# Kernel tuning notes

Measured on AMD Instinct MI355X. Metric: run time of the kernel, lower is better.

## Reference

```python
import jax, jax.numpy as jnp
import numpy as np

# ---- static config (decode path of PagedAttention) ----
B = 16            # batch (one new token per sequence in decode)
H = 32            # query heads
KVH = 8           # kv heads (GQA)
G = H // KVH      # query heads per kv head group
D = 128           # head dim (Rope hard-codes split at 64)
BLOCK = 16        # block_size hard-coded in forward
CACHE_LEN = 4096  # cache_length[b] for every b (uniform)
NUM_FETCH = CACHE_LEN // BLOCK          # 256 full blocks fetched per seq
MAX_BLOCKS = B * (NUM_FETCH + 1)        # 4112; one spare block per seq
ROWS = MAX_BLOCKS * BLOCK               # 65792 flat cache rows
SCALE = 1.0 / np.sqrt(D)                # softmax_scale


def setup_inputs() -> dict:
    key = jax.random.key(0)
    ks = jax.random.split(key, 6)
    Q = jax.random.normal(ks[0], (B, H, D), jnp.float32)
    K = jax.random.normal(ks[1], (B, KVH, D), jnp.float32)
    V = jax.random.normal(ks[2], (B, KVH, D), jnp.float32)
    Kcache = jax.random.normal(ks[3], (ROWS, KVH, D), jnp.float32)
    Vcache = jax.random.normal(ks[4], (ROWS, KVH, D), jnp.float32)
    # rotary cos/sin for the current decode position (one per sequence)
    inv_freq = 1.0 / (10000.0 ** (jnp.arange(D // 2, dtype=jnp.float32) / (D // 2)))
    pos = jnp.full((B, 1), float(CACHE_LEN), dtype=jnp.float32)
    ang = pos * inv_freq[None, :]                      # [B, 64]
    cos = jnp.concatenate([jnp.cos(ang), jnp.cos(ang)], axis=-1)  # [B, 128]
    sin = jnp.concatenate([jnp.sin(ang), jnp.sin(ang)], axis=-1)
    # block-aligned page table: seq b owns blocks [b*257, b*257+256)
    fetch_slots = ((jnp.arange(B, dtype=jnp.int32)[:, None] * (NUM_FETCH + 1)
                    + jnp.arange(NUM_FETCH, dtype=jnp.int32)[None, :]) * BLOCK)
    save_slots = ((jnp.arange(B, dtype=jnp.int32) * (NUM_FETCH + 1) + NUM_FETCH)
                  * BLOCK).reshape(B, 1)
    return dict(Q=Q, K=K, V=V, Kcache=Kcache, Vcache=Vcache,
                cos=cos, sin=sin, fetch_slots=fetch_slots, save_slots=save_slots)


def _rope(x, cos, sin):
    # x: [B, heads, 128]; matches torch: x*cos + concat(-x2, x1)*sin
    x1, x2 = x[..., :D // 2], x[..., D // 2:]
    rot = jnp.concatenate([-x2, x1], axis=-1)
    return x * cos[:, None, :] + rot * sin[:, None, :]


def reference(Q, K, V, Kcache, Vcache, cos, sin, fetch_slots, save_slots):
    Qr = _rope(Q, cos, sin)          # [B, H, D]
    Kr = _rope(K, cos, sin)          # [B, KVH, D]
    # cache physical per-block layout is [kv_heads, block, d]
    Kc4 = Kcache.reshape(MAX_BLOCKS, KVH, BLOCK, D)
    Vc4 = Vcache.reshape(MAX_BLOCKS, KVH, BLOCK, D)
    blk = fetch_slots // BLOCK                         # [B, NUM_FETCH]
    # paged gather: [B, NF, KVH, BLOCK, D] -> [B, KVH, CACHE_LEN, D]
    Kb = jnp.transpose(Kc4[blk], (0, 2, 1, 3, 4)).reshape(B, KVH, CACHE_LEN, D)
    Vb = jnp.transpose(Vc4[blk], (0, 2, 1, 3, 4)).reshape(B, KVH, CACHE_LEN, D)
    # append the new (roped) K and raw V token -> N = CACHE_LEN + 1
    Kall = jnp.concatenate([Kb, Kr[:, :, None, :]], axis=2)
    Vall = jnp.concatenate([Vb, V[:, :, None, :]], axis=2)
    # torch's tile-repeat maps query head h -> kv head h % KVH;
    # reshape [B, G, KVH, D] puts head g*KVH+k at [g, k], kv index k. Exact match.
    Qg = Qr.reshape(B, G, KVH, D)
    scores = jnp.einsum('bgkd,bknd->bgkn', Qg, Kall) * SCALE   # [B,G,KVH,N]
    p = jax.nn.softmax(scores, axis=-1)
    Yg = jnp.einsum('bgkn,bknd->bgkd', p, Vall)                # [B,G,KVH,D]
    Y = Yg.reshape(B, H, D)
    # scatter-write of new K/V into save_slots (in-place cache update in torch;
    # does not affect Y since save blocks are disjoint from fetch blocks)
    # Kc4.at[save_slots[:,0]//BLOCK, :, save_slots[:,0]%BLOCK, :].set(Kr)
    return Y


if __name__ == '__main__':
    out = reference(**setup_inputs())
    print(out.shape, out.dtype)
```

## Files before the change

kernel.cpp:

```cpp
#include <hip/hip_runtime.h>

#define NB 16
#define NH 32
#define NKVH 8
#define NG 4
#define ND 128
#define BLOCK 16
#define NUM_FETCH 256
#define NSPLIT 16
#define CHUNK 256
#define ITERS 32

static constexpr float SCALE_LOG2E = 0.08838834764831845f * 1.4426950408889634f;


__global__ __launch_bounds__(256, 4) void pa_main(
    const float* __restrict__ Q,
    const float* __restrict__ Kcache,
    const float* __restrict__ Vcache,
    const float* __restrict__ cosb,
    const float* __restrict__ sinb,
    const int*   __restrict__ fetch,
    float* __restrict__ accws,
    float* __restrict__ lws)
{
    const int wg    = blockIdx.x;
    const int split = wg & (NSPLIT - 1);
    const int kvh   = (wg >> 4) & (NKVH - 1);
    const int b     = wg >> 7;

    const int tid  = threadIdx.x;
    const int w    = tid >> 6;
    const int lane = tid & 63;
    const int half = lane >> 5;
    const int l32  = lane & 31;
    const int d0   = l32 << 2;

    const float4 cs = *(const float4*)(cosb + b * ND + d0);
    const float4 sn = *(const float4*)(sinb + b * ND + d0);
    const float  sgn = (d0 < 64) ? -1.f : 1.f;
    const int    dp  = d0 ^ 64;
    float qv[NG][4];
    #pragma unroll
    for (int g = 0; g < NG; ++g) {
        const float* qp = Q + (size_t)(b * NH + g * NKVH + kvh) * ND;
        const float4 qa = *(const float4*)(qp + d0);
        const float4 qb = *(const float4*)(qp + dp);
        qv[g][0] = (qa.x * cs.x + sgn * qb.x * sn.x) * SCALE_LOG2E;
        qv[g][1] = (qa.y * cs.y + sgn * qb.y * sn.y) * SCALE_LOG2E;
        qv[g][2] = (qa.z * cs.z + sgn * qb.z * sn.z) * SCALE_LOG2E;
        qv[g][3] = (qa.w * cs.w + sgn * qb.w * sn.w) * SCALE_LOG2E;
    }

    float acc[NG][4] = {{0.f,0.f,0.f,0.f},{0.f,0.f,0.f,0.f},
                        {0.f,0.f,0.f,0.f},{0.f,0.f,0.f,0.f}};
    float lsum[NG] = {0.f, 0.f, 0.f, 0.f};

    const int   pos0  = split * CHUNK + w * 2 + half;
    const int* __restrict__ fbase = fetch + b * NUM_FETCH;
    const size_t khead = (size_t)kvh * (BLOCK * ND);
    const float* kb = Kcache + khead + d0;
    const float* vb = Vcache + khead + d0;

    #pragma unroll 2
    for (int it = 0; it < ITERS; ++it) {
        const int pos = pos0 + it * 8;
        const size_t off = (size_t)fbase[pos >> 4] * (NKVH * ND)
                         + (size_t)(pos & (BLOCK - 1)) * ND;
        const float4 k4 = *(const float4*)(kb + off);
        const float4 v4 = *(const float4*)(vb + off);

        float s[NG];
        #pragma unroll
        for (int g = 0; g < NG; ++g)
            s[g] = qv[g][0]*k4.x + qv[g][1]*k4.y + qv[g][2]*k4.z + qv[g][3]*k4.w;

        #pragma unroll
        for (int m = 16; m >= 1; m >>= 1) {
            #pragma unroll
            for (int g = 0; g < NG; ++g)
                s[g] += __shfl_xor(s[g], m, 64);
        }

        #pragma unroll
        for (int g = 0; g < NG; ++g) {
            const float p = __builtin_amdgcn_exp2f(s[g]);
            lsum[g]   += p;
            acc[g][0] += p * v4.x;
            acc[g][1] += p * v4.y;
            acc[g][2] += p * v4.z;
            acc[g][3] += p * v4.w;
        }
    }

    #pragma unroll
    for (int g = 0; g < NG; ++g) {
        lsum[g] += __shfl_xor(lsum[g], 32, 64);
        #pragma unroll
        for (int j = 0; j < 4; ++j)
            acc[g][j] += __shfl_xor(acc[g][j], 32, 64);
    }

    __shared__ float s_acc[4][NG][ND];
    __shared__ float s_l[4][NG];
    if (half == 0) {
        #pragma unroll
        for (int g = 0; g < NG; ++g)
            *(float4*)&s_acc[w][g][d0] =
                make_float4(acc[g][0], acc[g][1], acc[g][2], acc[g][3]);
        if (l32 == 0) {
            #pragma unroll
            for (int g = 0; g < NG; ++g) s_l[w][g] = lsum[g];
        }
    }
    __syncthreads();

    const size_t pslot = (size_t)(b * NKVH + kvh) * NSPLIT + split;
    for (int idx = tid; idx < NG * ND; idx += 256) {
        const int g = idx >> 7, d = idx & 127;
        accws[(pslot * NG + g) * ND + d] =
            s_acc[0][g][d] + s_acc[1][g][d] + s_acc[2][g][d] + s_acc[3][g][d];
    }
    if (tid < NG)
        lws[pslot * NG + tid] = s_l[0][tid] + s_l[1][tid] + s_l[2][tid] + s_l[3][tid];
}

__global__ __launch_bounds__(128) void pa_combine(
    const float* __restrict__ Q,
    const float* __restrict__ Knew,
    const float* __restrict__ Vnew,
    const float* __restrict__ cosb,
    const float* __restrict__ sinb,
    const float* __restrict__ accws,
    const float* __restrict__ lws,
    float* __restrict__ Y)
{
    const int bh  = blockIdx.x;
    const int b   = bh >> 5;
    const int h   = bh & (NH - 1);
    const int kvh = h & (NKVH - 1);
    const int g   = h >> 3;
    const int d   = threadIdx.x;

    const float c   = cosb[b * ND + d];
    const float s   = sinb[b * ND + d];
    const float sgn = (d < 64) ? -1.f : 1.f;
    const int   dp  = d ^ 64;
    const float* qp = Q    + (size_t)(b * NH + h) * ND;
    const float* kp = Knew + (size_t)(b * NKVH + kvh) * ND;
    const float qr = qp[d] * c + sgn * qp[dp] * s;
    const float kr = kp[d] * c + sgn * kp[dp] * s;

    float prod = qr * kr;
    #pragma unroll
    for (int m = 32; m >= 1; m >>= 1) prod += __shfl_xor(prod, m, 64);
    __shared__ float red[2];
    if ((d & 63) == 0) red[d >> 6] = prod;
    __syncthreads();

    const float p = __builtin_amdgcn_exp2f((red[0] + red[1]) * SCALE_LOG2E);

    const size_t base = ((size_t)(b * NKVH + kvh) * NSPLIT) * NG + g;
    float acc = p * Vnew[(size_t)(b * NKVH + kvh) * ND + d];
    float lt  = p;
    #pragma unroll
    for (int sp = 0; sp < NSPLIT; ++sp) {
        acc += accws[(base + (size_t)sp * NG) * ND + d];
        lt  += lws[base + (size_t)sp * NG];
    }
    Y[(size_t)(b * NH + h) * ND + d] = acc / lt;
}

extern "C" void kernel_launch(void* const* d_in, const int* in_sizes, int n_in,
                              void* d_out, int out_size, void* d_ws, size_t ws_size,
                              hipStream_t stream)
{
    const float* Q    = (const float*)d_in[0];
    const float* K    = (const float*)d_in[1];
    const float* V    = (const float*)d_in[2];
    const float* Kc   = (const float*)d_in[3];
    const float* Vc   = (const float*)d_in[4];
    const float* cosb = (const float*)d_in[5];
    const float* sinb = (const float*)d_in[6];
    const int*   fetch = (const int*)d_in[7];

    float* accws = (float*)d_ws;
    float* lws   = accws + (size_t)NB * NKVH * NSPLIT * NG * ND;
    float* Y     = (float*)d_out;

    pa_main<<<NB * NKVH * NSPLIT, 256, 0, stream>>>(Q, Kc, Vc, cosb, sinb, fetch, accws, lws);
    pa_combine<<<NB * NH, 128, 0, stream>>>(Q, K, V, cosb, sinb, accws, lws, Y);
}
```

Before: 102.6 us.

## Software-pipeline paged K/V loads two pages ahead with scalar page indices

```diff
diff --git a/kernel.cpp b/kernel.cpp
--- a/kernel.cpp
+++ b/kernel.cpp
@@ -8,8 +8,7 @@
 #define BLOCK 16
 #define NUM_FETCH 256
 #define NSPLIT 16
-#define CHUNK 256
-#define ITERS 32
+#define PAGES_PER_WG 16
 
 static constexpr float SCALE_LOG2E = 0.08838834764831845f * 1.4426950408889634f;
 
@@ -36,6 +35,8 @@
     const int l32  = lane & 31;
     const int d0   = l32 << 2;
 
+    const int* fb = fetch + b * NUM_FETCH + split * PAGES_PER_WG;
+
     const float4 cs = *(const float4*)(cosb + b * ND + d0);
     const float4 sn = *(const float4*)(sinb + b * ND + d0);
     const float  sgn = (d0 < 64) ? -1.f : 1.f;
@@ -56,32 +57,22 @@
                         {0.f,0.f,0.f,0.f},{0.f,0.f,0.f,0.f}};
     float lsum[NG] = {0.f, 0.f, 0.f, 0.f};
 
-    const int   pos0  = split * CHUNK + w * 2 + half;
-    const int* __restrict__ fbase = fetch + b * NUM_FETCH;
+    const int sub = w * 2 + half;
     const size_t khead = (size_t)kvh * (BLOCK * ND);
-    const float* kb = Kcache + khead + d0;
-    const float* vb = Vcache + khead + d0;
-
-    #pragma unroll 2
-    for (int it = 0; it < ITERS; ++it) {
-        const int pos = pos0 + it * 8;
-        const size_t off = (size_t)fbase[pos >> 4] * (NKVH * ND)
-                         + (size_t)(pos & (BLOCK - 1)) * ND;
-        const float4 k4 = *(const float4*)(kb + off);
-        const float4 v4 = *(const float4*)(vb + off);
-
+    const float* kb = Kcache + khead + (size_t)sub * ND + d0;
+    const float* vb = Vcache + khead + (size_t)sub * ND + d0;
+
+    auto body = [&](const float4& k4, const float4& v4) {
         float s[NG];
         #pragma unroll
         for (int g = 0; g < NG; ++g)
             s[g] = qv[g][0]*k4.x + qv[g][1]*k4.y + qv[g][2]*k4.z + qv[g][3]*k4.w;
-
         #pragma unroll
         for (int m = 16; m >= 1; m >>= 1) {
             #pragma unroll
             for (int g = 0; g < NG; ++g)
                 s[g] += __shfl_xor(s[g], m, 64);
         }
-
         #pragma unroll
         for (int g = 0; g < NG; ++g) {
             const float p = __builtin_amdgcn_exp2f(s[g]);
@@ -91,6 +82,36 @@
             acc[g][2] += p * v4.z;
             acc[g][3] += p * v4.w;
         }
+    };
+
+    const int pgA = __builtin_amdgcn_readfirstlane(fb[0]);
+    const int pgB = __builtin_amdgcn_readfirstlane(fb[1]);
+    const size_t offA = (size_t)pgA * (NKVH * ND);
+    const size_t offB = (size_t)pgB * (NKVH * ND);
+    float4 kA0 = *(const float4*)(kb + offA);
+    float4 kA1 = *(const float4*)(kb + offA + 8 * ND);
+    float4 vA0 = *(const float4*)(vb + offA);
+    float4 vA1 = *(const float4*)(vb + offA + 8 * ND);
+    float4 kB0 = *(const float4*)(kb + offB);
+    float4 kB1 = *(const float4*)(kb + offB + 8 * ND);
+    float4 vB0 = *(const float4*)(vb + offB);
+    float4 vB1 = *(const float4*)(vb + offB + 8 * ND);
+
+    #pragma unroll 2
+    for (int j = 0; j < PAGES_PER_WG; ++j) {
+        const int jn = (j + 2 < PAGES_PER_WG) ? (j + 2) : (PAGES_PER_WG - 1);
+        const int pgC = __builtin_amdgcn_readfirstlane(fb[jn]);
+        const size_t offC = (size_t)pgC * (NKVH * ND);
+        const float4 kC0 = *(const float4*)(kb + offC);
+        const float4 kC1 = *(const float4*)(kb + offC + 8 * ND);
+        const float4 vC0 = *(const float4*)(vb + offC);
+        const float4 vC1 = *(const float4*)(vb + offC + 8 * ND);
+
+        body(kA0, vA0);
+        body(kA1, vA1);
+
+        kA0 = kB0; kA1 = kB1; vA0 = vB0; vA1 = vB1;
+        kB0 = kC0; kB1 = kC1; vB0 = vC0; vB1 = vC1;
     }
 
     #pragma unroll
```

After: 105.6 us. 2.9% more time.

## Restructure decode loop to page-major tiles with four rows per half-wave

Applied to the files above, without the earlier changes.

```diff
diff --git a/kernel.cpp b/kernel.cpp
--- a/kernel.cpp
+++ b/kernel.cpp
@@ -7,9 +7,9 @@
 #define ND 128
 #define BLOCK 16
 #define NUM_FETCH 256
-#define NSPLIT 16
-#define CHUNK 256
-#define ITERS 32
+#define NSPLIT 32
+#define PAGES_PER_WG 8
+#define ITERS 4
 
 static constexpr float SCALE_LOG2E = 0.08838834764831845f * 1.4426950408889634f;
 
@@ -26,8 +26,8 @@
 {
     const int wg    = blockIdx.x;
     const int split = wg & (NSPLIT - 1);
-    const int kvh   = (wg >> 4) & (NKVH - 1);
-    const int b     = wg >> 7;
+    const int kvh   = (wg >> 5) & (NKVH - 1);
+    const int b     = wg >> 8;
 
     const int tid  = threadIdx.x;
     const int w    = tid >> 6;
@@ -35,6 +35,10 @@
     const int half = lane >> 5;
     const int l32  = lane & 31;
     const int d0   = l32 << 2;
+
+    const int* fb = fetch + b * NUM_FETCH + split * PAGES_PER_WG;
+    const int  ps = w >> 1;
+    const int  r0 = ((w & 1) * 2 + half) * 4;
 
     const float4 cs = *(const float4*)(cosb + b * ND + d0);
     const float4 sn = *(const float4*)(sinb + b * ND + d0);
@@ -56,40 +60,57 @@
                         {0.f,0.f,0.f,0.f},{0.f,0.f,0.f,0.f}};
     float lsum[NG] = {0.f, 0.f, 0.f, 0.f};
 
-    const int   pos0  = split * CHUNK + w * 2 + half;
-    const int* __restrict__ fbase = fetch + b * NUM_FETCH;
-    const size_t khead = (size_t)kvh * (BLOCK * ND);
-    const float* kb = Kcache + khead + d0;
-    const float* vb = Vcache + khead + d0;
-
-    #pragma unroll 2
-    for (int it = 0; it < ITERS; ++it) {
-        const int pos = pos0 + it * 8;
-        const size_t off = (size_t)fbase[pos >> 4] * (NKVH * ND)
-                         + (size_t)(pos & (BLOCK - 1)) * ND;
-        const float4 k4 = *(const float4*)(kb + off);
-        const float4 v4 = *(const float4*)(vb + off);
-
-        float s[NG];
-        #pragma unroll
-        for (int g = 0; g < NG; ++g)
-            s[g] = qv[g][0]*k4.x + qv[g][1]*k4.y + qv[g][2]*k4.z + qv[g][3]*k4.w;
+    const size_t gbase = (size_t)kvh * (BLOCK * ND) + (size_t)r0 * ND + d0;
+    const float* kb = Kcache + gbase;
+    const float* vb = Vcache + gbase;
+
+    int pgNext = fb[ps];
+
+    #pragma unroll 1
+    for (int i = 0; i < ITERS; ++i) {
+        const int pg = __builtin_amdgcn_readfirstlane(pgNext);
+        const int ni = (i + 1 < ITERS) ? (i + 1) * 2 + ps : ps;
+        pgNext = fb[ni];
+
+        const size_t off = (size_t)pg * (NKVH * ND);
+        const float4 k0 = *(const float4*)(kb + off);
+        const float4 k1 = *(const float4*)(kb + off + 1 * ND);
+        const float4 k2 = *(const float4*)(kb + off + 2 * ND);
+        const float4 k3 = *(const float4*)(kb + off + 3 * ND);
+        const float4 v0 = *(const float4*)(vb + off);
+        const float4 v1 = *(const float4*)(vb + off + 1 * ND);
+        const float4 v2 = *(const float4*)(vb + off + 2 * ND);
+        const float4 v3 = *(const float4*)(vb + off + 3 * ND);
+
+        float s[4][NG];
+        #pragma unroll
+        for (int g = 0; g < NG; ++g) {
+            s[0][g] = qv[g][0]*k0.x + qv[g][1]*k0.y + qv[g][2]*k0.z + qv[g][3]*k0.w;
+            s[1][g] = qv[g][0]*k1.x + qv[g][1]*k1.y + qv[g][2]*k1.z + qv[g][3]*k1.w;
+            s[2][g] = qv[g][0]*k2.x + qv[g][1]*k2.y + qv[g][2]*k2.z + qv[g][3]*k2.w;
+            s[3][g] = qv[g][0]*k3.x + qv[g][1]*k3.y + qv[g][2]*k3.z + qv[g][3]*k3.w;
+        }
 
         #pragma unroll
         for (int m = 16; m >= 1; m >>= 1) {
             #pragma unroll
-            for (int g = 0; g < NG; ++g)
-                s[g] += __shfl_xor(s[g], m, 64);
+            for (int r = 0; r < 4; ++r)
+                #pragma unroll
+                for (int g = 0; g < NG; ++g)
+                    s[r][g] += __shfl_xor(s[r][g], m, 64);
         }
 
         #pragma unroll
         for (int g = 0; g < NG; ++g) {
-            const float p = __builtin_amdgcn_exp2f(s[g]);
-            lsum[g]   += p;
-            acc[g][0] += p * v4.x;
-            acc[g][1] += p * v4.y;
-            acc[g][2] += p * v4.z;
-            acc[g][3] += p * v4.w;
+            const float p0 = __builtin_amdgcn_exp2f(s[0][g]);
+            const float p1 = __builtin_amdgcn_exp2f(s[1][g]);
+            const float p2 = __builtin_amdgcn_exp2f(s[2][g]);
+            const float p3 = __builtin_amdgcn_exp2f(s[3][g]);
+            lsum[g] += (p0 + p1) + (p2 + p3);
+            acc[g][0] += p0 * v0.x + p1 * v1.x + p2 * v2.x + p3 * v3.x;
+            acc[g][1] += p0 * v0.y + p1 * v1.y + p2 * v2.y + p3 * v3.y;
+            acc[g][2] += p0 * v0.z + p1 * v1.z + p2 * v2.z + p3 * v3.z;
+            acc[g][3] += p0 * v0.w + p1 * v1.w + p2 * v2.w + p3 * v3.w;
         }
     }
 
```

Result: slower. 118.3 us (+15.3%).
